# Kernel tuning notes

Hardware: AMD Instinct MI355X
Metric: run time of the kernel (lower is better)

Reference implementation:

```python
import jax, jax.numpy as jnp
import numpy as np

N_NODES = 40000
N_EDGES = 150000
H, D = 4, 128  # heads, per-head dim (h_feats=512)


def _edge_softmax(e, dst, n):
    # e: [E, H] attention logits; softmax over edges sharing a dst node
    m = jax.ops.segment_max(e, dst, num_segments=n)
    w = jnp.exp(e - m[dst])
    s = jax.ops.segment_sum(w, dst, num_segments=n)
    return w / s[dst]


def _gat_conv(x, src, dst, W, al, ar, b, activate):
    # DGL GATConv: feat = x @ W -> [N, H, D]
    n = x.shape[0]
    feat = (x @ W).reshape(n, H, D)
    el = jnp.einsum('nhd,hd->nh', feat, al)  # [N, H]
    er = jnp.einsum('nhd,hd->nh', feat, ar)
    e = jax.nn.leaky_relu(el[src] + er[dst], negative_slope=0.2)  # [E, H]
    a = _edge_softmax(e, dst, n)
    msg = feat[src] * a[:, :, None]  # [E, H, D]
    out = jax.ops.segment_sum(msg, dst, num_segments=n)  # [N, H, D]
    out = out + b.reshape(1, H, D)
    if activate:
        out = jax.nn.leaky_relu(out, negative_slope=0.01)  # F.leaky_relu default
    return out


def _hetero_layer(h, edges, W, al, ar, b, activate):
    # HeteroGraphConv with aggregate='sum' over edge types, then flatten heads
    n = h.shape[0]
    out = jnp.zeros((n, H, D), h.dtype)
    for t, (src, dst) in enumerate(edges):
        out = out + _gat_conv(h, src, dst, W[t], al[t], ar[t], b[t], activate)
    return out.reshape(n, H * D)


def setup_inputs() -> dict:
    key = jax.random.key(0)
    ks = jax.random.split(key, 20)
    inp = {}
    inp['x'] = jax.random.normal(ks[0], (N_NODES, 1024), jnp.float32)
    for i, nm in enumerate(['src0', 'dst0', 'src1', 'dst1']):
        inp[nm] = jax.random.randint(ks[1 + i], (N_EDGES,), 0, N_NODES, jnp.int32)
    def wscale(k, shape, fan_in):
        return jax.random.normal(k, shape, jnp.float32) * (1.0 / np.sqrt(fan_in))
    inp['W0'] = wscale(ks[5], (2, 1024, 512), 1024)
    inp['al0'] = wscale(ks[6], (2, H, D), D)
    inp['ar0'] = wscale(ks[7], (2, H, D), D)
    inp['b0'] = jnp.zeros((2, 512), jnp.float32)
    inp['W1'] = wscale(ks[8], (2, 512, 512), 512)
    inp['al1'] = wscale(ks[9], (2, H, D), D)
    inp['ar1'] = wscale(ks[10], (2, H, D), D)
    inp['b1'] = jnp.zeros((2, 512), jnp.float32)
    inp['W2'] = wscale(ks[11], (2, 512, 512), 512)
    inp['al2'] = wscale(ks[12], (2, H, D), D)
    inp['ar2'] = wscale(ks[13], (2, H, D), D)
    inp['b2'] = jnp.zeros((2, 512), jnp.float32)
    inp['Wout'] = wscale(ks[14], (512, 2983), 512)
    inp['bout'] = jnp.zeros((2983,), jnp.float32)
    return inp


def reference(x, src0, dst0, src1, dst1,
              W0, al0, ar0, b0, W1, al1, ar1, b1, W2, al2, ar2, b2,
              Wout, bout):
    edges = [(src0, dst0), (src1, dst1)]
    h = _hetero_layer(x, edges, W0, al0, ar0, b0, activate=True)
    h = _hetero_layer(h, edges, W1, al1, ar1, b1, activate=True)
    h = _hetero_layer(h, edges, W2, al2, ar2, b2, activate=False)
    return h @ Wout + bout
```

## Files before the change

kernel.cpp:

```cpp
#include <hip/hip_runtime.h>
#include <hip/hip_bf16.h>

#define NN 40000
#define NE 150000
#define HF 512
#define NHEAD 4

typedef __bf16 bf16x8 __attribute__((ext_vector_type(8)));
typedef float floatx4 __attribute__((ext_vector_type(4)));
typedef __hip_bfloat16 bf16;
typedef unsigned short u16;

__device__ __forceinline__ float bf2f(bf16 v) { return __bfloat162float(v); }

__global__ void cast_k(const float* __restrict__ in, bf16* __restrict__ out, int n) {
    int i = (blockIdx.x * blockDim.x + threadIdx.x) * 8;
    if (i + 7 < n) {
        float4 v0 = *(const float4*)(in + i);
        float4 v1 = *(const float4*)(in + i + 4);
        union { uint4 u; u16 s[8]; } w;
        float fv[8] = {v0.x, v0.y, v0.z, v0.w, v1.x, v1.y, v1.z, v1.w};
#pragma unroll
        for (int j = 0; j < 8; j++) {
            bf16 b = __float2bfloat16(fv[j]);
            w.s[j] = *(const u16*)&b;
        }
        *(uint4*)(out + i) = w.u;
    } else {
        for (int j = i; j < n; j++) out[j] = __float2bfloat16(in[j]);
    }
}

__global__ void transpose_k(const float* __restrict__ W, bf16* __restrict__ WT,
                            int K, int Nn) {
    __shared__ float tile[32][33];
    int n0 = blockIdx.x * 32, k0 = blockIdx.y * 32;
    int tx = threadIdx.x, ty = threadIdx.y;
    int n = n0 + tx, k = k0 + ty;
    if (n < Nn && k < K) tile[ty][tx] = W[(size_t)k * Nn + n];
    __syncthreads();
    int nn = n0 + ty, kk = k0 + tx;
    if (nn < Nn && kk < K) WT[(size_t)nn * K + kk] = __float2bfloat16(tile[tx][ty]);
}

template <bool HAS_BIAS>
__global__ __launch_bounds__(256) void gemm_k(const bf16* __restrict__ A,
                                              const bf16* __restrict__ BT,
                                              float* __restrict__ C,
                                              const float* __restrict__ bias,
                                              int M, int Nn, int K) {
    __shared__ __align__(16) unsigned short As[128][40];
    __shared__ __align__(16) unsigned short Bs[128][40];

    const int nwg = gridDim.x * gridDim.y;
    const int orig = blockIdx.y * gridDim.x + blockIdx.x;
    const int qq = nwg >> 3, r8 = nwg & 7;
    const int xcd = orig & 7, loc = orig >> 3;
    const int swz = (xcd < r8 ? xcd * (qq + 1) : r8 * (qq + 1) + (xcd - r8) * qq) + loc;
    const int ntile = swz % gridDim.x;
    const int mtile = swz / gridDim.x;
    const int m0 = mtile * 128;
    const int n0 = ntile * 128;

    const int t = threadIdx.x;
    const int lane = t & 63;
    const int wave = t >> 6;
    const int wm = wave >> 1, wn = wave & 1;
    const int q = lane >> 4, r = lane & 15;

    const int srow = t >> 1;
    const int scol = (t & 1) << 4;
    const int arow = m0 + srow;
    const int brow = n0 + srow;
    const bool a_ok = arow < M;
    const bool b_ok = brow < Nn;
    const unsigned short* Arow = (const unsigned short*)A + (size_t)arow * K + scol;
    const unsigned short* Brow = (const unsigned short*)BT + (size_t)brow * K + scol;

    floatx4 acc[4][4] = {};
    for (int k0 = 0; k0 < K; k0 += 32) {
        uint4 av0 = make_uint4(0, 0, 0, 0), av1 = av0, bv0 = av0, bv1 = av0;
        if (a_ok) {
            av0 = *(const uint4*)(Arow + k0);
            av1 = *(const uint4*)(Arow + k0 + 8);
        }
        if (b_ok) {
            bv0 = *(const uint4*)(Brow + k0);
            bv1 = *(const uint4*)(Brow + k0 + 8);
        }
        *(uint4*)&As[srow][scol] = av0;
        *(uint4*)&As[srow][scol + 8] = av1;
        *(uint4*)&Bs[srow][scol] = bv0;
        *(uint4*)&Bs[srow][scol + 8] = bv1;
        __syncthreads();
        bf16x8 a[4], b[4];
#pragma unroll
        for (int i = 0; i < 4; i++) a[i] = *(const bf16x8*)&As[wm * 64 + i * 16 + r][q * 8];
#pragma unroll
        for (int j = 0; j < 4; j++) b[j] = *(const bf16x8*)&Bs[wn * 64 + j * 16 + r][q * 8];
#pragma unroll
        for (int i = 0; i < 4; i++)
#pragma unroll
            for (int j = 0; j < 4; j++)
                acc[i][j] = __builtin_amdgcn_mfma_f32_16x16x32_bf16(a[i], b[j], acc[i][j], 0, 0, 0);
        __syncthreads();
    }
#pragma unroll
    for (int i = 0; i < 4; i++)
#pragma unroll
        for (int j = 0; j < 4; j++)
#pragma unroll
            for (int rr = 0; rr < 4; rr++) {
                int row = m0 + wm * 64 + i * 16 + q * 4 + rr;
                int col = n0 + wn * 64 + j * 16 + r;
                if (row < M && col < Nn) {
                    float v = acc[i][j][rr];
                    if (HAS_BIAS) v += bias[col];
                    C[(size_t)row * Nn + col] = v;
                }
            }
}

__global__ void attn_k(const float* __restrict__ feat, const float* __restrict__ al,
                       const float* __restrict__ ar, float* __restrict__ el,
                       float* __restrict__ er) {
    int lane = threadIdx.x & 63;
    int wave = threadIdx.x >> 6;
    int node = blockIdx.x * 4 + wave;
    if (node >= NN) return;
    int h = lane >> 4;
    const float* fp = feat + (size_t)node * HF + lane * 8;
    float4 f0 = *(const float4*)fp;
    float4 f1 = *(const float4*)(fp + 4);
    const float* alp = al + h * 128 + (lane & 15) * 8;
    const float* arp = ar + h * 128 + (lane & 15) * 8;
    float fv[8] = {f0.x, f0.y, f0.z, f0.w, f1.x, f1.y, f1.z, f1.w};
    float sl = 0.f, sr = 0.f;
#pragma unroll
    for (int j = 0; j < 8; j++) {
        sl += fv[j] * alp[j];
        sr += fv[j] * arp[j];
    }
#pragma unroll
    for (int off = 8; off >= 1; off >>= 1) {
        sl += __shfl_down(sl, off, 16);
        sr += __shfl_down(sr, off, 16);
    }
    if ((lane & 15) == 0) {
        el[node * NHEAD + h] = sl;
        er[node * NHEAD + h] = sr;
    }
}

__global__ void deg_count_k(const int* __restrict__ dst, int* __restrict__ deg) {
    int e = blockIdx.x * blockDim.x + threadIdx.x;
    if (e < NE) atomicAdd(&deg[dst[e]], 1);
}

__global__ void scan_k(const int* __restrict__ deg, int* __restrict__ off) {
    __shared__ int part[1024];
    const int CH = (NN + 1023) >> 10;
    int t = threadIdx.x;
    int base = t * CH;
    int s = 0;
    for (int i = 0; i < CH; i++) {
        int idx = base + i;
        if (idx < NN) s += deg[idx];
    }
    part[t] = s;
    __syncthreads();
    for (int d = 1; d < 1024; d <<= 1) {
        int v = (t >= d) ? part[t - d] : 0;
        __syncthreads();
        part[t] += v;
        __syncthreads();
    }
    int run = (t == 0) ? 0 : part[t - 1];
    for (int i = 0; i < CH; i++) {
        int idx = base + i;
        if (idx < NN) {
            off[idx] = run;
            run += deg[idx];
        } else if (idx == NN) {
            off[NN] = run;
        }
    }
}

__global__ void fill_k(const int* __restrict__ src, const int* __restrict__ dst,
                       const int* __restrict__ off, int* __restrict__ cur,
                       int* __restrict__ csrc) {
    int e = blockIdx.x * blockDim.x + threadIdx.x;
    if (e >= NE) return;
    int d = dst[e];
    int p = atomicAdd(&cur[d], 1);
    csrc[off[d] + p] = src[e];
}

__global__ __launch_bounds__(256) void gather_k(
    const int* __restrict__ off, const int* __restrict__ csrc,
    const float* __restrict__ el, const float* __restrict__ er,
    const float* __restrict__ feat, const float* __restrict__ bt,
    bf16* __restrict__ hout, int first, int act) {
    int lane = threadIdx.x & 63;
    int wave = threadIdx.x >> 6;
    int d = blockIdx.x * 4 + wave;
    if (d >= NN) return;
    int h = lane >> 4;
    int o0 = off[d], o1 = off[d + 1];
    float erd = er[d * NHEAD + h];

    float m = -3.0e38f;
    for (int i = o0; i < o1; i++) {
        int s = csrc[i];
        float lg = el[s * NHEAD + h] + erd;
        lg = lg > 0.f ? lg : 0.2f * lg;
        m = fmaxf(m, lg);
    }
    float sum = 0.f;
    for (int i = o0; i < o1; i++) {
        int s = csrc[i];
        float lg = el[s * NHEAD + h] + erd;
        lg = lg > 0.f ? lg : 0.2f * lg;
        sum += __expf(lg - m);
    }
    float inv = sum > 0.f ? 1.f / sum : 0.f;
    float acc[8] = {};
    for (int i = o0; i < o1; i++) {
        int s = csrc[i];
        float lg = el[s * NHEAD + h] + erd;
        lg = lg > 0.f ? lg : 0.2f * lg;
        float a = __expf(lg - m) * inv;
        const float* fp = feat + (size_t)s * HF + lane * 8;
        float4 f0 = *(const float4*)fp;
        float4 f1 = *(const float4*)(fp + 4);
        acc[0] += f0.x * a;
        acc[1] += f0.y * a;
        acc[2] += f0.z * a;
        acc[3] += f0.w * a;
        acc[4] += f1.x * a;
        acc[5] += f1.y * a;
        acc[6] += f1.z * a;
        acc[7] += f1.w * a;
    }
    const float* bp = bt + lane * 8;
    float4 b0 = *(const float4*)bp;
    float4 b1 = *(const float4*)(bp + 4);
    float bv[8] = {b0.x, b0.y, b0.z, b0.w, b1.x, b1.y, b1.z, b1.w};
    u16* hp = (u16*)(hout + (size_t)d * HF + lane * 8);
    union U8 { uint4 v; u16 s[8]; };
    U8 prev;
    if (!first) prev.v = *(const uint4*)hp;
    U8 outw;
#pragma unroll
    for (int j = 0; j < 8; j++) {
        float v = acc[j] + bv[j];
        if (act) v = v > 0.f ? v : 0.01f * v;
        if (!first) {
            bf16 pb = *(const bf16*)&prev.s[j];
            v += bf2f(pb);
        }
        bf16 ob = __float2bfloat16(v);
        outw.s[j] = *(const u16*)&ob;
    }
    *(uint4*)hp = outw.v;
}

extern "C" void kernel_launch(void* const* d_in, const int* in_sizes, int n_in,
                              void* d_out, int out_size, void* d_ws, size_t ws_size,
                              hipStream_t stream) {
    const float* x = (const float*)d_in[0];
    const int* srcs[2] = {(const int*)d_in[1], (const int*)d_in[3]};
    const int* dsts[2] = {(const int*)d_in[2], (const int*)d_in[4]};
    const float* W[3] = {(const float*)d_in[5], (const float*)d_in[9], (const float*)d_in[13]};
    const float* al[3] = {(const float*)d_in[6], (const float*)d_in[10], (const float*)d_in[14]};
    const float* ar[3] = {(const float*)d_in[7], (const float*)d_in[11], (const float*)d_in[15]};
    const float* bb[3] = {(const float*)d_in[8], (const float*)d_in[12], (const float*)d_in[16]};
    const float* Wout = (const float*)d_in[17];
    const float* bout = (const float*)d_in[18];

    char* ws = (char*)d_ws;
    size_t off = 0;
    auto walloc = [&](size_t bytes) {
        void* p = ws + off;
        off = (off + bytes + 255) & ~(size_t)255;
        return p;
    };
    bf16* h0 = (bf16*)walloc((size_t)NN * HF * 2);
    bf16* h1 = (bf16*)walloc((size_t)NN * HF * 2);
    float* feat = (float*)walloc((size_t)NN * HF * 4);
    float* el = (float*)walloc((size_t)NN * NHEAD * 4);
    float* er = (float*)walloc((size_t)NN * NHEAD * 4);
    bf16* WT = (bf16*)walloc((size_t)2983 * 512 * 2);
    int* deg = (int*)walloc((size_t)NN * 4);
    int* cur = (int*)walloc((size_t)NN * 4);
    int* offs[2];
    int* csrc[2];
    for (int t = 0; t < 2; t++) {
        offs[t] = (int*)walloc((size_t)(NN + 1) * 4);
        csrc[t] = (int*)walloc((size_t)NE * 4);
    }

    bf16* xb = (bf16*)((char*)d_out + (size_t)NN * HF * 4);

    cast_k<<<(NN * 1024 / 8 + 255) / 256, 256, 0, stream>>>(x, xb, NN * 1024);

    const int EB = (NE + 255) / 256;
    for (int t = 0; t < 2; t++) {
        hipMemsetAsync(deg, 0, (size_t)NN * 4, stream);
        hipMemsetAsync(cur, 0, (size_t)NN * 4, stream);
        deg_count_k<<<EB, 256, 0, stream>>>(dsts[t], deg);
        scan_k<<<1, 1024, 0, stream>>>(deg, offs[t]);
        fill_k<<<EB, 256, 0, stream>>>(srcs[t], dsts[t], offs[t], cur, csrc[t]);
    }

    const int MT = (NN + 127) / 128;

    for (int l = 0; l < 3; l++) {
        const int K = (l == 0) ? 1024 : 512;
        const bf16* hin = (l == 0) ? xb : ((l == 1) ? h0 : h1);
        bf16* hout = (l == 0) ? h0 : ((l == 1) ? h1 : h0);
        const int act = (l < 2) ? 1 : 0;
        for (int t = 0; t < 2; t++) {
            transpose_k<<<dim3(512 / 32, K / 32), dim3(32, 32), 0, stream>>>(
                W[l] + (size_t)t * K * 512, WT, K, 512);
            gemm_k<false><<<dim3(512 / 128, MT), 256, 0, stream>>>(
                hin, WT, feat, nullptr, NN, 512, K);
            attn_k<<<NN / 4, 256, 0, stream>>>(feat, al[l] + t * HF, ar[l] + t * HF, el, er);
            gather_k<<<NN / 4, 256, 0, stream>>>(offs[t], csrc[t], el, er, feat,
                                                 bb[l] + t * HF, hout, t == 0 ? 1 : 0, act);
        }
    }

    transpose_k<<<dim3((2983 + 31) / 32, 512 / 32), dim3(32, 32), 0, stream>>>(
        Wout, WT, 512, 2983);
    gemm_k<true><<<dim3((2983 + 127) / 128, MT), 256, 0, stream>>>(
        h0, WT, (float*)d_out, bout, NN, 2983, 512);
}
```

Baseline: 1.811 ms.

## Load GEMM tiles directly to LDS and use online softmax in gather

The GEMM tile loads now use global_load_lds (direct global-to-LDS DMA) instead of staging through registers. This drops the LDS padding and clamps out-of-range rows instead of zero-filling them. Separately, the gather kernel merges the max and sum passes into one online-softmax pass, saving one sweep over the neighbor list. The unpadded LDS layout may add bank conflicts on the MFMA fragment reads, and the online softmax adds extra exp calls per edge.

```diff
diff --git a/kernel.cpp b/kernel.cpp
--- a/kernel.cpp
+++ b/kernel.cpp
@@ -12,6 +12,12 @@
 typedef unsigned short u16;
 
 __device__ __forceinline__ float bf2f(bf16 v) { return __bfloat162float(v); }
+
+__device__ __forceinline__ void gload16(const void* g, void* l) {
+    __builtin_amdgcn_global_load_lds(
+        (const __attribute__((address_space(1))) void*)g,
+        (__attribute__((address_space(3))) void*)l, 16, 0, 0);
+}
 
 __global__ void cast_k(const float* __restrict__ in, bf16* __restrict__ out, int n) {
     int i = (blockIdx.x * blockDim.x + threadIdx.x) * 8;
@@ -49,8 +55,8 @@
                                               float* __restrict__ C,
                                               const float* __restrict__ bias,
                                               int M, int Nn, int K) {
-    __shared__ __align__(16) unsigned short As[128][40];
-    __shared__ __align__(16) unsigned short Bs[128][40];
+    __shared__ __align__(16) unsigned short As[128][32];
+    __shared__ __align__(16) unsigned short Bs[128][32];
 
     const int nwg = gridDim.x * gridDim.y;
     const int orig = blockIdx.y * gridDim.x + blockIdx.x;
@@ -68,30 +74,27 @@
     const int wm = wave >> 1, wn = wave & 1;
     const int q = lane >> 4, r = lane & 15;
 
-    const int srow = t >> 1;
-    const int scol = (t & 1) << 4;
-    const int arow = m0 + srow;
-    const int brow = n0 + srow;
-    const bool a_ok = arow < M;
-    const bool b_ok = brow < Nn;
-    const unsigned short* Arow = (const unsigned short*)A + (size_t)arow * K + scol;
-    const unsigned short* Brow = (const unsigned short*)BT + (size_t)brow * K + scol;
+    const int srow = wave * 32 + (lane >> 2);
+    const int scol = (lane & 3) * 8;
+    int ar0 = m0 + srow;        if (ar0 >= M)  ar0 = M - 1;
+    int ar1 = m0 + srow + 16;   if (ar1 >= M)  ar1 = M - 1;
+    int br0 = n0 + srow;        if (br0 >= Nn) br0 = Nn - 1;
+    int br1 = n0 + srow + 16;   if (br1 >= Nn) br1 = Nn - 1;
+    const unsigned short* Ag0 = (const unsigned short*)A + (size_t)ar0 * K + scol;
+    const unsigned short* Ag1 = (const unsigned short*)A + (size_t)ar1 * K + scol;
+    const unsigned short* Bg0 = (const unsigned short*)BT + (size_t)br0 * K + scol;
+    const unsigned short* Bg1 = (const unsigned short*)BT + (size_t)br1 * K + scol;
+    unsigned short* Al0 = &As[0][0] + wave * 1024;
+    unsigned short* Al1 = Al0 + 512;
+    unsigned short* Bl0 = &Bs[0][0] + wave * 1024;
+    unsigned short* Bl1 = Bl0 + 512;
 
     floatx4 acc[4][4] = {};
     for (int k0 = 0; k0 < K; k0 += 32) {
-        uint4 av0 = make_uint4(0, 0, 0, 0), av1 = av0, bv0 = av0, bv1 = av0;
-        if (a_ok) {
-            av0 = *(const uint4*)(Arow + k0);
-            av1 = *(const uint4*)(Arow + k0 + 8);
-        }
-        if (b_ok) {
-            bv0 = *(const uint4*)(Brow + k0);
-            bv1 = *(const uint4*)(Brow + k0 + 8);
-        }
-        *(uint4*)&As[srow][scol] = av0;
-        *(uint4*)&As[srow][scol + 8] = av1;
-        *(uint4*)&Bs[srow][scol] = bv0;
-        *(uint4*)&Bs[srow][scol + 8] = bv1;
+        gload16(Ag0 + k0, Al0);
+        gload16(Ag1 + k0, Al1);
+        gload16(Bg0 + k0, Bl0);
+        gload16(Bg1 + k0, Bl1);
         __syncthreads();
         bf16x8 a[4], b[4];
 #pragma unroll
@@ -210,19 +213,14 @@
     int o0 = off[d], o1 = off[d + 1];
     float erd = er[d * NHEAD + h];
 
-    float m = -3.0e38f;
+    float m = -3.0e38f, sum = 0.f;
     for (int i = o0; i < o1; i++) {
         int s = csrc[i];
         float lg = el[s * NHEAD + h] + erd;
         lg = lg > 0.f ? lg : 0.2f * lg;
-        m = fmaxf(m, lg);
-    }
-    float sum = 0.f;
-    for (int i = o0; i < o1; i++) {
-        int s = csrc[i];
-        float lg = el[s * NHEAD + h] + erd;
-        lg = lg > 0.f ? lg : 0.2f * lg;
-        sum += __expf(lg - m);
+        float mn = fmaxf(m, lg);
+        sum = sum * __expf(m - mn) + __expf(lg - mn);
+        m = mn;
     }
     float inv = sum > 0.f ? 1.f / sum : 0.f;
     float acc[8] = {};
```

Measured after the change: 1.764 ms. -2.6%, faster.
